# Kernel tuning notes

Hardware: AMD Instinct MI355X
Metric: run time of the kernel (lower is better)

## Reference

```python
import jax, jax.numpy as jnp
import numpy as np

TEMPERATURE = 0.5
B, D = 4096, 256


def setup_inputs() -> dict:
    key = jax.random.key(0)
    k1, k2 = jax.random.split(key)
    emb_i = jax.random.normal(k1, (B, D), dtype=jnp.float32)
    emb_j = jax.random.normal(k2, (B, D), dtype=jnp.float32)
    return {"emb_i": emb_i, "emb_j": emb_j}


def reference(emb_i, emb_j):
    # NT-Xent (SimCLR) loss, vectorized version of the per-sample python loop.
    n = emb_i.shape[0]
    eps = 1e-12
    z_i = emb_i / jnp.maximum(jnp.linalg.norm(emb_i, axis=1, keepdims=True), eps)
    z_j = emb_j / jnp.maximum(jnp.linalg.norm(emb_j, axis=1, keepdims=True), eps)
    reps = jnp.concatenate([z_i, z_j], axis=0)               # [2N, D], unit rows
    # cosine similarity of unit vectors == dot product
    sim = reps @ reps.T                                       # [2N, 2N]
    exp_sim = jnp.exp(sim / TEMPERATURE)
    # denominator for row i: sum over k != i of exp(sim[i,k]/T)
    denom = jnp.sum(exp_sim, axis=1) - jnp.diagonal(exp_sim)  # [2N]
    # positive-pair sims: sim[k, k+N] and sim[k+N, k]
    pos = jnp.concatenate([jnp.diagonal(sim[:n, n:]), jnp.diagonal(sim[n:, :n])])
    # l_ij = log(exp(pos/T) / denom) = pos/T - log(denom)
    loss_terms = pos / TEMPERATURE - jnp.log(denom)
    return (1.0 / (2 * n)) * jnp.sum(loss_terms)
```

## Files before the change

### kernel.cpp

```cpp
#include <hip/hip_runtime.h>
#include <math.h>


#define NROWS 8192
#define NHALF 4096
#define DIM   256
#define BM    128
#define BN    128
#define BK    64
#define NCB   (NROWS / BN)
#define NTRI  (NCB * (NCB + 1) / 2)

typedef __attribute__((ext_vector_type(8))) short bf16x8;
typedef __attribute__((ext_vector_type(4))) float f32x4;

static __device__ __forceinline__ unsigned short f2bf(float x) {
  unsigned int u = __float_as_uint(x);
  unsigned int r = (u + 0x7FFFu + ((u >> 16) & 1u)) >> 16;
  return (unsigned short)r;
}

__global__ __launch_bounds__(256) void normalize_kernel(
    const float* __restrict__ emb_i, const float* __restrict__ emb_j,
    unsigned short* __restrict__ zb, float* __restrict__ out) {
  if (blockIdx.x == 0 && threadIdx.x == 0) out[0] = 0.f;
  int w = threadIdx.x >> 6, lane = threadIdx.x & 63;
  int row = blockIdx.x * 4 + w;
  const float* src = (row < NHALF) ? (emb_i + (size_t)row * DIM)
                                   : (emb_j + (size_t)(row - NHALF) * DIM);
  float4 v = ((const float4*)src)[lane];
  float ss = v.x * v.x + v.y * v.y + v.z * v.z + v.w * v.w;
  #pragma unroll
  for (int off = 32; off; off >>= 1) ss += __shfl_down(ss, off, 64);
  float total = __shfl(ss, 0, 64);
  float inv = 1.0f / fmaxf(sqrtf(total), 1e-12f);
  ushort4 o;
  o.x = f2bf(v.x * inv); o.y = f2bf(v.y * inv);
  o.z = f2bf(v.z * inv); o.w = f2bf(v.w * inv);
  ((ushort4*)&zb[(size_t)row * DIM])[lane] = o;
}

__global__ __launch_bounds__(256) void denom_kernel(
    const unsigned short* __restrict__ zb, float* __restrict__ denomP,
    float* __restrict__ posv) {
  __shared__ unsigned short As[BM * BK];
  __shared__ unsigned short Bs[BN * BK];

  int t = blockIdx.x;
  int by = (int)((sqrtf(8.0f * (float)t + 1.0f) - 1.0f) * 0.5f);
  while ((by + 1) * (by + 2) / 2 <= t) ++by;
  while (by * (by + 1) / 2 > t) --by;
  int bx = t - by * (by + 1) / 2;

  const int tid = threadIdx.x;
  const int w = tid >> 6;
  const int lane = tid & 63;
  const int wr = w >> 1, wc = w & 1;
  const int quad = lane >> 4;
  const int m16 = lane & 15;
  const int row0 = bx * BM;
  const int col0 = by * BN;

  f32x4 acc[4][4];
  #pragma unroll
  for (int i = 0; i < 4; ++i)
    #pragma unroll
    for (int j = 0; j < 4; ++j) {
      f32x4 z4 = {0.f, 0.f, 0.f, 0.f};
      acc[i][j] = z4;
    }

  for (int kc = 0; kc < DIM; kc += BK) {
    #pragma unroll
    for (int tt = 0; tt < 4; ++tt) {
      int rbase = w * 32 + tt * 8;
      int gr = rbase + (lane >> 3);
      int gk = kc + (lane & 7) * 8;
      __builtin_amdgcn_global_load_lds(
          (const __attribute__((address_space(1))) unsigned int*)
              &zb[(size_t)(row0 + gr) * DIM + gk],
          (__attribute__((address_space(3))) unsigned int*)&As[rbase * BK],
          16, 0, 0);
      __builtin_amdgcn_global_load_lds(
          (const __attribute__((address_space(1))) unsigned int*)
              &zb[(size_t)(col0 + gr) * DIM + gk],
          (__attribute__((address_space(3))) unsigned int*)&Bs[rbase * BK],
          16, 0, 0);
    }
    __syncthreads();

    #pragma unroll
    for (int ks = 0; ks < BK; ks += 32) {
      bf16x8 af[4], bfr[4];
      #pragma unroll
      for (int i = 0; i < 4; ++i)
        af[i] = *(const bf16x8*)&As[(wr * 64 + i * 16 + m16) * BK + ks + quad * 8];
      #pragma unroll
      for (int j = 0; j < 4; ++j)
        bfr[j] = *(const bf16x8*)&Bs[(wc * 64 + j * 16 + m16) * BK + ks + quad * 8];
      #pragma unroll
      for (int i = 0; i < 4; ++i)
        #pragma unroll
        for (int j = 0; j < 4; ++j)
          acc[i][j] = __builtin_amdgcn_mfma_f32_16x16x32_bf16(
              af[i], bfr[j], acc[i][j], 0, 0, 0);
    }
    __syncthreads();
  }

  if (col0 - row0 == NHALF) {
    #pragma unroll
    for (int i = 0; i < 4; ++i)
      #pragma unroll
      for (int j = 0; j < 4; ++j) {
        int gcol = col0 + wc * 64 + j * 16 + m16;
        #pragma unroll
        for (int r = 0; r < 4; ++r) {
          int grow = row0 + wr * 64 + i * 16 + quad * 4 + r;
          if (gcol - grow == NHALF) posv[grow] = acc[i][j][r];
        }
      }
  }

  float rs[4][4];
  float cs[4] = {0.f, 0.f, 0.f, 0.f};
  #pragma unroll
  for (int i = 0; i < 4; ++i)
    #pragma unroll
    for (int r = 0; r < 4; ++r) rs[i][r] = 0.f;

  #pragma unroll
  for (int i = 0; i < 4; ++i)
    #pragma unroll
    for (int j = 0; j < 4; ++j) {
      int gcol = col0 + wc * 64 + j * 16 + m16;
      #pragma unroll
      for (int r = 0; r < 4; ++r) {
        int grow = row0 + wr * 64 + i * 16 + quad * 4 + r;
        float e = (grow == gcol) ? 0.f : __expf(2.0f * acc[i][j][r]);
        rs[i][r] += e;
        cs[j] += e;
      }
    }

  float* red = (float*)As;

  #pragma unroll
  for (int i = 0; i < 4; ++i)
    #pragma unroll
    for (int r = 0; r < 4; ++r) {
      float v = rs[i][r];
      v += __shfl_xor(v, 1, 16);
      v += __shfl_xor(v, 2, 16);
      v += __shfl_xor(v, 4, 16);
      v += __shfl_xor(v, 8, 16);
      if (m16 == 0) red[wc * 128 + wr * 64 + i * 16 + quad * 4 + r] = v;
    }
  #pragma unroll
  for (int j = 0; j < 4; ++j) {
    float v = cs[j];
    v += __shfl_xor(v, 16, 64);
    v += __shfl_xor(v, 32, 64);
    if (quad == 0) red[256 + wr * 128 + wc * 64 + j * 16 + m16] = v;
  }
  __syncthreads();

  if (tid < 128) {
    denomP[(size_t)by * NROWS + row0 + tid] = red[tid] + red[128 + tid];
  } else if (bx != by) {
    int c = tid - 128;
    denomP[(size_t)bx * NROWS + col0 + c] = red[256 + c] + red[384 + c];
  }
}

__global__ __launch_bounds__(256) void reduce_kernel(
    const float* __restrict__ denomP, const float* __restrict__ posv,
    float* __restrict__ out) {
  int tid = threadIdx.x;
  int r = blockIdx.x * 256 + tid;
  float s = 0.f;
  #pragma unroll 8
  for (int b = 0; b < NCB; ++b) s += denomP[(size_t)b * NROWS + r];
  float v = -logf(s);
  if (r < NHALF) v += 4.0f * posv[r];
  #pragma unroll
  for (int off = 32; off; off >>= 1) v += __shfl_down(v, off, 64);
  __shared__ float s4[4];
  if ((tid & 63) == 0) s4[tid >> 6] = v;
  __syncthreads();
  if (tid == 0)
    atomicAdd(out, (s4[0] + s4[1] + s4[2] + s4[3]) * (1.0f / 8192.0f));
}

extern "C" void kernel_launch(void* const* d_in, const int* in_sizes, int n_in,
                              void* d_out, int out_size, void* d_ws,
                              size_t ws_size, hipStream_t stream) {
  const float* emb_i = (const float*)d_in[0];
  const float* emb_j = (const float*)d_in[1];
  unsigned short* zb = (unsigned short*)d_ws;
  float* denomP = (float*)(zb + (size_t)NROWS * DIM);
  float* posv = denomP + (size_t)NCB * NROWS;
  float* out = (float*)d_out;

  normalize_kernel<<<NROWS / 4, 256, 0, stream>>>(emb_i, emb_j, zb, out);
  denom_kernel<<<NTRI, 256, 0, stream>>>(zb, denomP, posv);
  reduce_kernel<<<NROWS / 256, 256, 0, stream>>>(denomP, posv, out);
}
```

Baseline: 111.0 us.

## Store LDS tiles in MFMA fragment order and fold exp scale into normalization

Rearranges the shared-memory layout so each 16x32 MFMA operand fragment is stored contiguously, letting each lane read its bf16x8 with a linear address instead of a row-strided one that likely causes LDS bank conflicts. It also pre-scales the normalized embeddings by sqrt(2/ln2) so the exponent becomes a bare exp2, and rescales the positive term to match. The scaling changes bf16 rounding slightly.

```diff
diff --git a/kernel.cpp b/kernel.cpp
--- a/kernel.cpp
+++ b/kernel.cpp
@@ -11,8 +11,17 @@
 #define NCB   (NROWS / BN)
 #define NTRI  (NCB * (NCB + 1) / 2)
 
+#define SCALE    1.69864344f
+#define POSMUL   1.38629436f
+
 typedef __attribute__((ext_vector_type(8))) short bf16x8;
 typedef __attribute__((ext_vector_type(4))) float f32x4;
+
+#if __has_builtin(__builtin_amdgcn_exp2f)
+#define EXP2(x) __builtin_amdgcn_exp2f(x)
+#else
+#define EXP2(x) __expf((x) * 0.69314718f)
+#endif
 
 static __device__ __forceinline__ unsigned short f2bf(float x) {
   unsigned int u = __float_as_uint(x);
@@ -33,7 +42,7 @@
   #pragma unroll
   for (int off = 32; off; off >>= 1) ss += __shfl_down(ss, off, 64);
   float total = __shfl(ss, 0, 64);
-  float inv = 1.0f / fmaxf(sqrtf(total), 1e-12f);
+  float inv = SCALE / fmaxf(sqrtf(total), 1e-12f);
   ushort4 o;
   o.x = f2bf(v.x * inv); o.y = f2bf(v.y * inv);
   o.z = f2bf(v.z * inv); o.w = f2bf(v.w * inv);
@@ -43,8 +52,8 @@
 __global__ __launch_bounds__(256) void denom_kernel(
     const unsigned short* __restrict__ zb, float* __restrict__ denomP,
     float* __restrict__ posv) {
-  __shared__ unsigned short As[BM * BK];
-  __shared__ unsigned short Bs[BN * BK];
+  __shared__ __attribute__((aligned(16))) unsigned short As[16 * 512];
+  __shared__ __attribute__((aligned(16))) unsigned short Bs[16 * 512];
 
   int t = blockIdx.x;
   int by = (int)((sqrtf(8.0f * (float)t + 1.0f) - 1.0f) * 0.5f);
@@ -72,32 +81,33 @@
 
   for (int kc = 0; kc < DIM; kc += BK) {
     #pragma unroll
-    for (int tt = 0; tt < 4; ++tt) {
-      int rbase = w * 32 + tt * 8;
-      int gr = rbase + (lane >> 3);
-      int gk = kc + (lane & 7) * 8;
+    for (int t4 = 0; t4 < 4; ++t4) {
+      int ra = w * 4 + t4;
+      int grow = (ra >> 1) * 16 + m16;
+      int gk = kc + (ra & 1) * 32 + quad * 8;
       __builtin_amdgcn_global_load_lds(
           (const __attribute__((address_space(1))) unsigned int*)
-              &zb[(size_t)(row0 + gr) * DIM + gk],
-          (__attribute__((address_space(3))) unsigned int*)&As[rbase * BK],
+              &zb[(size_t)(row0 + grow) * DIM + gk],
+          (__attribute__((address_space(3))) unsigned int*)&As[ra * 512],
           16, 0, 0);
       __builtin_amdgcn_global_load_lds(
           (const __attribute__((address_space(1))) unsigned int*)
-              &zb[(size_t)(col0 + gr) * DIM + gk],
-          (__attribute__((address_space(3))) unsigned int*)&Bs[rbase * BK],
+              &zb[(size_t)(col0 + grow) * DIM + gk],
+          (__attribute__((address_space(3))) unsigned int*)&Bs[ra * 512],
           16, 0, 0);
     }
     __syncthreads();
 
     #pragma unroll
     for (int ks = 0; ks < BK; ks += 32) {
+      const int kst = ks >> 5;
       bf16x8 af[4], bfr[4];
       #pragma unroll
       for (int i = 0; i < 4; ++i)
-        af[i] = *(const bf16x8*)&As[(wr * 64 + i * 16 + m16) * BK + ks + quad * 8];
+        af[i] = *(const bf16x8*)&As[(wr * 8 + i * 2 + kst) * 512 + lane * 8];
       #pragma unroll
       for (int j = 0; j < 4; ++j)
-        bfr[j] = *(const bf16x8*)&Bs[(wc * 64 + j * 16 + m16) * BK + ks + quad * 8];
+        bfr[j] = *(const bf16x8*)&Bs[(wc * 8 + j * 2 + kst) * 512 + lane * 8];
       #pragma unroll
       for (int i = 0; i < 4; ++i)
         #pragma unroll
@@ -137,7 +147,7 @@
       #pragma unroll
       for (int r = 0; r < 4; ++r) {
         int grow = row0 + wr * 64 + i * 16 + quad * 4 + r;
-        float e = (grow == gcol) ? 0.f : __expf(2.0f * acc[i][j][r]);
+        float e = (grow == gcol) ? 0.f : EXP2(acc[i][j][r]);
         rs[i][r] += e;
         cs[j] += e;
       }
@@ -182,7 +192,7 @@
   #pragma unroll 8
   for (int b = 0; b < NCB; ++b) s += denomP[(size_t)b * NROWS + r];
   float v = -logf(s);
-  if (r < NHALF) v += 4.0f * posv[r];
+  if (r < NHALF) v += POSMUL * posv[r];
   #pragma unroll
   for (int off = 32; off; off >>= 1) v += __shfl_down(v, off, 64);
   __shared__ float s4[4];
```

New measurement: 116.8 us. 5.2% more time.
